# Performance work log

Hardware: AMD Instinct MI355X
Metric: run time of the kernel (lower is better)

Reference implementation:

```python
import jax, jax.numpy as jnp
import numpy as np

B, L, DIN, D, H, NL, DFF = 4, 1024, 64, 512, 8, 3, 2048
DH = D // H
N_RBF = 8
LARGE_NEG, CLAMP = 10000.0, 20.0


def layernorm(x, g, b, eps=1e-5):
    m = x.mean(-1, keepdims=True)
    v = x.var(-1, keepdims=True)
    return (x - m) * jax.lax.rsqrt(v + eps) * g + b


def sinusoidal_pe(length, d):
    pos = np.arange(length, dtype=np.float32)[:, None]
    div = np.exp(np.arange(0, d, 2, dtype=np.float32) * (-np.log(10000.0) / d))
    pe = np.zeros((length, d), dtype=np.float32)
    pe[:, 0::2] = np.sin(pos * div)
    pe[:, 1::2] = np.cos(pos * div)
    return jnp.asarray(pe)


def rbf(v):
    centers = jnp.linspace(0.0, 1.0, N_RBF)
    widths = jnp.full((N_RBF,), 0.2)
    diff = (v[..., None] - centers) / (widths + 1e-6)
    return jnp.exp(-0.5 * diff * diff)


def setup_inputs() -> dict:
    key = jax.random.key(0)
    ks = jax.random.split(key, 40)
    g = lambda k, shape: (jax.random.normal(k, shape) * 0.02).astype(jnp.float32)
    feat_dim = D + 2 + 2 * N_RBF  # base PE + raw(2) + 2 RBFs
    inp = {
        "x": jax.random.normal(ks[0], (B, L, DIN), jnp.float32),
        "lengths": jax.random.randint(ks[1], (B,), L // 2, L + 1),
        "input_delay": jax.random.uniform(ks[2], (B,), jnp.float32),
        "c_local": jax.random.uniform(ks[3], (B, L), jnp.float32).at[:, 0].set(0.0),
        "c_sink": jax.random.uniform(ks[4], (B, L), jnp.float32),
        # input projection
        "in_w": g(ks[5], (D, DIN)), "in_b": jnp.zeros((D,)),
        # delay encoder: Linear(1,D) -> GELU -> Linear(D,D) -> LN
        "de_w1": g(ks[6], (D, 1)), "de_b1": jnp.zeros((D,)),
        "de_w2": g(ks[7], (D, D)), "de_b2": jnp.zeros((D,)),
        "de_ln_g": jnp.ones((D,)), "de_ln_b": jnp.zeros((D,)),
        # corr positional encoding
        "cpe_w": g(ks[8], (D, feat_dim)), "cpe_b": jnp.zeros((D,)),
        "cpe_ln_g": jnp.ones((D,)), "cpe_ln_b": jnp.zeros((D,)),
        "gain": jnp.float32(0.5),
        # bias params
        "alpha": jnp.float32(10.0), "beta": jnp.float32(10.0),
        "floor": jnp.float32(0.1), "gamma": jnp.float32(0.7),
        # per-layer stacks
        "inproj_w": g(ks[9], (NL, 3 * D, D)), "inproj_b": jnp.zeros((NL, 3 * D)),
        "outproj_w": g(ks[10], (NL, D, D)), "outproj_b": jnp.zeros((NL, D)),
        "ln1_g": jnp.ones((NL, D)), "ln1_b": jnp.zeros((NL, D)),
        "ln2_g": jnp.ones((NL, D)), "ln2_b": jnp.zeros((NL, D)),
        "ff_w1": g(ks[11], (NL, DFF, D)), "ff_b1": jnp.zeros((NL, DFF)),
        "ff_w2": g(ks[12], (NL, D, DFF)), "ff_b2": jnp.zeros((NL, D)),
        "out_ln_g": jnp.ones((D,)), "out_ln_b": jnp.zeros((D,)),
    }
    return inp


def _forward(x, input_delay, c_local, c_sink, in_w, in_b, de_w1, de_b1, de_w2, de_b2,
             de_ln_g, de_ln_b, cpe_w, cpe_b, cpe_ln_g, cpe_ln_b, gain, alpha, beta,
             floor, gamma, inproj_w, inproj_b, outproj_w, outproj_b, ln1_g, ln1_b,
             ln2_g, ln2_b, ff_w1, ff_b1, ff_w2, ff_b2, out_ln_g, out_ln_b, lengths):
    Bc, Lc, _ = x.shape
    mask = jnp.arange(Lc)[None, :] >= lengths[:, None]          # [B,L] True=pad

    # input projection
    h = x @ in_w.T + in_b

    # delay feature encoder
    e = input_delay[:, None] @ de_w1.T + de_b1
    e = jax.nn.gelu(e, approximate=False) @ de_w2.T + de_b2
    e = layernorm(e, de_ln_g, de_ln_b)
    h = h + e[:, None, :]

    # corr positional encoding (uses clamped correlations)
    cl = jnp.clip(c_local, 0.0, 1.0)
    cs = jnp.clip(c_sink, 0.0, 1.0)
    pe_base = jnp.broadcast_to(sinusoidal_pe(Lc, D)[None], (Bc, Lc, D))
    z = jnp.concatenate([pe_base, jnp.stack([cl, cs], -1), rbf(cl), rbf(cs)], axis=-1)
    pe = layernorm(z @ cpe_w.T + cpe_b, cpe_ln_g, cpe_ln_b)
    pe = gain * pe
    pe = jnp.where(mask[..., None], 0.0, pe)
    h = h + pe

    # neighbor-correlation attention bias [B,1,L,L] (identical across layers/heads)
    idx = jnp.arange(Lc)
    neigh = jnp.abs(idx[None, :] - idx[:, None]) == 1           # [L,L]
    c_edge = jnp.zeros((Bc, Lc, Lc), x.dtype)
    c_edge = c_edge.at[:, 1:, :-1].set(jnp.broadcast_to(c_local[:, 1:, None], (Bc, Lc - 1, Lc - 1)))
    c_edge = c_edge.at[:, :-1, 1:].set(jnp.broadcast_to(c_local[:, None, 1:], (Bc, Lc - 1, Lc - 1)))
    bias = alpha * jnp.where(neigh[None], c_edge, 0.0)
    bias = jnp.where(mask[:, :, None] | mask[:, None, :], 0.0, bias)

    # sink bias (row 0 only): floor + (1-floor)*(c_sink^gamma)
    c_remap = floor + (1.0 - floor) * jnp.power(cs + 1e-6, gamma)
    sink_row = beta * jnp.where(mask, 0.0, c_remap)             # [B,L]
    attn_bias = bias[:, None].at[:, :, 0, :].add(sink_row[:, None, :])  # [B,1,L,L]

    pad = mask[:, None, None, :].astype(x.dtype)                # [B,1,1,L]
    scale = 1.0 / (DH ** 0.5)

    for i in range(NL):
        hn = layernorm(h, ln1_g[i], ln1_b[i])
        qkv = hn @ inproj_w[i].T + inproj_b[i]                  # [B,L,3D]
        q, k, v = jnp.split(qkv, 3, axis=-1)
        q = q.reshape(Bc, Lc, H, DH).transpose(0, 2, 1, 3)      # [B,H,L,d]
        k = k.reshape(Bc, Lc, H, DH).transpose(0, 2, 1, 3)
        v = v.reshape(Bc, Lc, H, DH).transpose(0, 2, 1, 3)
        scores = jnp.einsum('bhqd,bhkd->bhqk', q, k) * scale + attn_bias
        scores = scores - LARGE_NEG * pad
        scores = scores - scores.max(axis=-1, keepdims=True)
        scores = jnp.clip(scores, -CLAMP, CLAMP)
        attn = jax.nn.softmax(scores, axis=-1)
        o = jnp.einsum('bhqk,bhkd->bhqd', attn, v)
        o = o.transpose(0, 2, 1, 3).reshape(Bc, Lc, D)
        h = h + (o @ outproj_w[i].T + outproj_b[i])
        hn2 = layernorm(h, ln2_g[i], ln2_b[i])
        ff = jax.nn.gelu(hn2 @ ff_w1[i].T + ff_b1[i], approximate=False)
        h = h + (ff @ ff_w2[i].T + ff_b2[i])

    return layernorm(h, out_ln_g, out_ln_b)


def reference(x, lengths, input_delay, c_local, c_sink, in_w, in_b, de_w1, de_b1,
              de_w2, de_b2, de_ln_g, de_ln_b, cpe_w, cpe_b, cpe_ln_g, cpe_ln_b, gain,
              alpha, beta, floor, gamma, inproj_w, inproj_b, outproj_w, outproj_b,
              ln1_g, ln1_b, ln2_g, ln2_b, ff_w1, ff_b1, ff_w2, ff_b2, out_ln_g, out_ln_b):
    return _forward(x, input_delay, c_local, c_sink, in_w, in_b, de_w1, de_b1, de_w2,
                    de_b2, de_ln_g, de_ln_b, cpe_w, cpe_b, cpe_ln_g, cpe_ln_b, gain,
                    alpha, beta, floor, gamma, inproj_w, inproj_b, outproj_w,
                    outproj_b, ln1_g, ln1_b, ln2_g, ln2_b, ff_w1, ff_b1, ff_w2, ff_b2,
                    out_ln_g, out_ln_b, lengths)
```

## Files before the change

kernel.cpp:

```cpp
#include <hip/hip_runtime.h>
#include <math.h>

#define BB 4
#define LL 1024
#define DIN 64
#define DD 512
#define HH 8
#define DH 64
#define NLAYER 3
#define DFF 2048
#define FEAT 530
#define FEATP 544
#define MM 4096

typedef float f32x4 __attribute__((ext_vector_type(4)));
typedef short s16x8 __attribute__((ext_vector_type(8)));

__device__ __forceinline__ unsigned short f2bf(float f) {
    unsigned int u = __float_as_uint(f);
    u += 0x7fffu + ((u >> 16) & 1u);
    return (unsigned short)(u >> 16);
}
__device__ __forceinline__ float bf2f(unsigned short u) {
    return __uint_as_float(((unsigned int)u) << 16);
}
__device__ __forceinline__ float gelu_exact(float x) {
    return 0.5f * x * (1.0f + erff(x * 0.7071067811865475f));
}
__device__ __forceinline__ float wave_reduce_sum(float v) {
    #pragma unroll
    for (int o = 32; o; o >>= 1) v += __shfl_down(v, o);
    return v;
}
__device__ __forceinline__ void gload16(const unsigned short* g, unsigned short* l) {
    __builtin_amdgcn_global_load_lds(
        (const __attribute__((address_space(1))) unsigned int*)g,
        (__attribute__((address_space(3))) unsigned int*)l, 16, 0, 0);
}

__global__ __launch_bounds__(256) void cvt_kernel(
    const float* __restrict__ in, unsigned short* __restrict__ out, int n)
{
    for (int i = blockIdx.x * 256 + threadIdx.x; i < n; i += gridDim.x * 256)
        out[i] = f2bf(in[i]);
}

__global__ __launch_bounds__(256) void cpe_pad_kernel(
    const float* __restrict__ in, unsigned short* __restrict__ out)
{
    for (int i = blockIdx.x * 256 + threadIdx.x; i < DD * FEATP; i += gridDim.x * 256) {
        int r = i / FEATP, c = i - r * FEATP;
        out[i] = (c < FEAT) ? f2bf(in[(size_t)r * FEAT + c]) : 0;
    }
}

__global__ __launch_bounds__(256) void build_z_kernel(
    const float* __restrict__ c_local, const float* __restrict__ c_sink,
    unsigned short* __restrict__ Z)
{
    int row = blockIdx.x;
    int b = row >> 10, l = row & 1023;
    int t = threadIdx.x;
    unsigned short* zr = Z + (size_t)row * FEATP;
    for (int d = t; d < DD; d += 256) {
        int i = d >> 1;
        float dv = expf((float)(2 * i) * (-0.017988946135618352f));
        float ang = (float)l * dv;
        zr[d] = f2bf((d & 1) ? cosf(ang) : sinf(ang));
    }
    if (t < 32) {
        float cl = c_local[(size_t)b * LL + l]; cl = fminf(fmaxf(cl, 0.f), 1.f);
        float cs = c_sink [(size_t)b * LL + l]; cs = fminf(fmaxf(cs, 0.f), 1.f);
        float v = 0.f;
        if (t == 0) v = cl;
        else if (t == 1) v = cs;
        else if (t < 10)  { float c = (float)(t - 2) * (1.0f / 7.0f);  float df = (cl - c) / 0.200001f; v = expf(-0.5f * df * df); }
        else if (t < 18)  { float c = (float)(t - 10) * (1.0f / 7.0f); float df = (cs - c) / 0.200001f; v = expf(-0.5f * df * df); }
        zr[512 + t] = (t < 18) ? f2bf(v) : 0;
    }
}

__global__ __launch_bounds__(256) void sink_kernel(
    const float* __restrict__ c_sink, const int* __restrict__ lengths,
    const float* __restrict__ beta_p, const float* __restrict__ floor_p,
    const float* __restrict__ gamma_p, float* __restrict__ srow)
{
    int i = blockIdx.x * 256 + threadIdx.x;
    int b = i >> 10, k = i & 1023;
    float beta = *beta_p, flr = *floor_p, gmm = *gamma_p;
    float cs = c_sink[i]; cs = fminf(fmaxf(cs, 0.f), 1.f);
    float v = beta * (flr + (1.f - flr) * powf(cs + 1e-6f, gmm));
    srow[i] = (k < lengths[b]) ? v : 0.f;
}

__global__ __launch_bounds__(512) void delay_kernel(
    const float* __restrict__ delay, const float* __restrict__ w1, const float* __restrict__ b1,
    const float* __restrict__ w2, const float* __restrict__ b2,
    const float* __restrict__ lng, const float* __restrict__ lnb,
    float* __restrict__ e)
{
    int b = blockIdx.x;
    int t = threadIdx.x;
    __shared__ float g1[DD];
    __shared__ float red[16];
    float t1 = delay[b] * w1[t] + b1[t];
    g1[t] = gelu_exact(t1);
    __syncthreads();
    const float* wr = w2 + (size_t)t * DD;
    float s = b2[t];
    for (int j = 0; j < DD; j += 4) {
        float4 w4 = *(const float4*)(wr + j);
        s += w4.x * g1[j] + w4.y * g1[j+1] + w4.z * g1[j+2] + w4.w * g1[j+3];
    }
    float rs = wave_reduce_sum(s);
    float rss = wave_reduce_sum(s * s);
    int lane = t & 63, w = t >> 6;
    if (lane == 0) { red[w] = rs; red[8 + w] = rss; }
    __syncthreads();
    float mean = 0.f, msq = 0.f;
    #pragma unroll
    for (int i = 0; i < 8; ++i) { mean += red[i]; msq += red[8 + i]; }
    mean *= (1.0f / DD); msq *= (1.0f / DD);
    float rstd = rsqrtf(msq - mean * mean + 1e-5f);
    e[(size_t)b * DD + t] = (s - mean) * rstd * lng[t] + lnb[t];
}

template<int BM, int BN, int FM, int FN, int WGN, int MODE>
__global__ __launch_bounds__(256) void gemm_t(
    const unsigned short* __restrict__ A, const unsigned short* __restrict__ W,
    const float* __restrict__ bias, const float* __restrict__ resid,
    float* __restrict__ outf, unsigned short* __restrict__ outb,
    int M, int N, int K)
{
    __shared__ __align__(16) unsigned short As[BM * 32];
    __shared__ __align__(16) unsigned short Ws[BN * 32];
    int bm = blockIdx.y * BM, bn = blockIdx.x * BN;
    int t = threadIdx.x;
    int lane = t & 63, wid = t >> 6;
    int wr = wid / WGN, wc = wid % WGN;
    int l15 = lane & 15, lg = lane >> 4;
    int srow = lane >> 2;
    int sc8 = ((lane & 3) ^ ((lane >> 2) & 3) ^ ((lane >> 4) & 3)) * 8;
    int chunk8 = (lg ^ (l15 & 3) ^ ((l15 >> 2) & 3)) * 8;

    f32x4 acc[FM][FN] = {};
    int nk = K >> 5;

    for (int ks = 0; ks < nk; ++ks) {
        int kb = ks * 32;
        #pragma unroll
        for (int i = 0; i < BM / 64; ++i) {
            int row = wid * (BM / 4) + i * 16 + srow;
            gload16(A + (size_t)(bm + row) * K + kb + sc8, &As[(wid * (BM / 64) + i) * 512]);
        }
        #pragma unroll
        for (int i = 0; i < BN / 64; ++i) {
            int row = wid * (BN / 4) + i * 16 + srow;
            gload16(W + (size_t)(bn + row) * K + kb + sc8, &Ws[(wid * (BN / 64) + i) * 512]);
        }
        __syncthreads();
        s16x8 af[FM], wf[FN];
        #pragma unroll
        for (int mi = 0; mi < FM; ++mi)
            af[mi] = *(const s16x8*)&As[(wr * FM * 16 + mi * 16 + l15) * 32 + chunk8];
        #pragma unroll
        for (int ni = 0; ni < FN; ++ni)
            wf[ni] = *(const s16x8*)&Ws[(wc * FN * 16 + ni * 16 + l15) * 32 + chunk8];
        #pragma unroll
        for (int mi = 0; mi < FM; ++mi)
            #pragma unroll
            for (int ni = 0; ni < FN; ++ni)
                acc[mi][ni] = __builtin_amdgcn_mfma_f32_16x16x32_bf16(af[mi], wf[ni], acc[mi][ni], 0, 0, 0);
        __syncthreads();
    }

    int rbase = (lane >> 4) * 4;
    #pragma unroll
    for (int mi = 0; mi < FM; ++mi) {
        #pragma unroll
        for (int ni = 0; ni < FN; ++ni) {
            int n = bn + wc * FN * 16 + ni * 16 + l15;
            float bz = bias[n];
            #pragma unroll
            for (int r2 = 0; r2 < 4; ++r2) {
                int m = bm + wr * FM * 16 + mi * 16 + rbase + r2;
                float v = acc[mi][ni][r2] + bz;
                size_t o = (size_t)m * N + n;
                if (MODE == 0)      outf[o] = v;
                else if (MODE == 1) outb[o] = f2bf(v);
                else if (MODE == 2) outf[o] = v + resid[o];
                else                outb[o] = f2bf(gelu_exact(v));
            }
        }
    }
}

__global__ __launch_bounds__(256) void vtrans_kernel(
    const unsigned short* __restrict__ qkv, unsigned short* __restrict__ Vt)
{
    __shared__ unsigned short Ts[64 * 68];
    int l0 = blockIdx.x * 64;
    int hh = blockIdx.y;
    int b  = blockIdx.z;
    int t  = threadIdx.x;
    #pragma unroll
    for (int u = 0; u < 2; ++u) {
        int idx = t + u * 256;
        int r = idx >> 3, c8 = idx & 7;
        uint4 v = *(const uint4*)(qkv + (size_t)(b * LL + l0 + r) * 1536 + 1024 + hh * DH + c8 * 8);
        *(uint4*)&Ts[r * 68 + c8 * 8] = v;
    }
    __syncthreads();
    #pragma unroll
    for (int u = 0; u < 2; ++u) {
        int d = (t >> 3) + u * 32;
        int c = t & 7;
        unsigned short tmp[8];
        #pragma unroll
        for (int j = 0; j < 8; ++j) tmp[j] = Ts[(c * 8 + j) * 68 + d];
        *(uint4*)(Vt + ((size_t)((b * HH + hh) * DH + d)) * LL + l0 + c * 8) = *(const uint4*)tmp;
    }
}

#define SK 72
#define SPB 72
__global__ __launch_bounds__(256) void attn_mfma(
    const unsigned short* __restrict__ qkv, const unsigned short* __restrict__ Vt,
    const float* __restrict__ c_local, const float* __restrict__ srow,
    const int* __restrict__ lengths,
    const float* __restrict__ alpha_p,
    unsigned short* __restrict__ o)
{
    __shared__ __align__(16) unsigned short Ks[64 * SK];
    __shared__ __align__(16) unsigned short Vts[64 * SK];
    __shared__ __align__(16) unsigned short Psb[64 * SPB];

    int id = blockIdx.x;
    int swz = (id & 7) * 64 + (id >> 3);
    int q0 = (swz & 15) * 64;
    int hh = (swz >> 4) & 7;
    int b  = swz >> 7;

    int t  = threadIdx.x;
    int lane = t & 63, w = t >> 6;
    int l15 = lane & 15, lg = lane >> 4;
    int len = lengths[b];
    int nt = (len + 63) >> 6;
    const float alpha = *alpha_p;

    const unsigned short* qrow = qkv + (size_t)(b * LL + q0 + w * 16 + l15) * 1536 + hh * DH;
    s16x8 qf0 = *(const s16x8*)(qrow + lg * 8);
    s16x8 qf1 = *(const s16x8*)(qrow + 32 + lg * 8);
    #pragma unroll
    for (int j = 0; j < 8; ++j) {
        qf0[j] = (short)f2bf(bf2f((unsigned short)qf0[j]) * 0.125f);
        qf1[j] = (short)f2bf(bf2f((unsigned short)qf1[j]) * 0.125f);
    }

    float cm1[4], cp1[4];
    #pragma unroll
    for (int r2 = 0; r2 < 4; ++r2) {
        int qi = q0 + w * 16 + lg * 4 + r2;
        cm1[r2] = 0.f; cp1[r2] = 0.f;
        if (qi >= 1 && qi < len) {
            int src = (qi == 1 || qi == LL - 1) ? qi : qi - 1;
            cm1[r2] = alpha * c_local[(size_t)b * LL + src];
        }
        if (qi + 1 < LL && qi < len)
            cp1[r2] = alpha * c_local[(size_t)b * LL + qi + 1];
    }
    bool need_sink = (q0 == 0 && w == 0 && lg == 0);

    float m_run[4], l_run[4];
    f32x4 accO[4] = {};
    #pragma unroll
    for (int r2 = 0; r2 < 4; ++r2) { m_run[r2] = -1e30f; l_run[r2] = 0.f; }

    int sr = t >> 3, sc8 = (t & 7) * 8;
    const unsigned short* kbase = qkv + (size_t)(b * LL) * 1536 + 512 + hh * DH;
    const unsigned short* vbase = Vt + ((size_t)((b * HH + hh) * DH)) * LL;

    uint4 pk0 = *(const uint4*)(kbase + (size_t)sr * 1536 + sc8);
    uint4 pk1 = *(const uint4*)(kbase + (size_t)(sr + 32) * 1536 + sc8);
    uint4 pv0 = *(const uint4*)(vbase + (size_t)sr * LL + sc8);
    uint4 pv1 = *(const uint4*)(vbase + (size_t)(sr + 32) * LL + sc8);

    for (int kt = 0; kt < nt; ++kt) {
        int k0 = kt * 64;
        *(uint4*)&Ks[sr * SK + sc8]         = pk0;
        *(uint4*)&Ks[(sr + 32) * SK + sc8]  = pk1;
        *(uint4*)&Vts[sr * SK + sc8]        = pv0;
        *(uint4*)&Vts[(sr + 32) * SK + sc8] = pv1;
        if (kt + 1 < nt) {
            int kn = k0 + 64;
            pk0 = *(const uint4*)(kbase + (size_t)(kn + sr) * 1536 + sc8);
            pk1 = *(const uint4*)(kbase + (size_t)(kn + sr + 32) * 1536 + sc8);
            pv0 = *(const uint4*)(vbase + (size_t)sr * LL + kn + sc8);
            pv1 = *(const uint4*)(vbase + (size_t)(sr + 32) * LL + kn + sc8);
        }
        __syncthreads();

        f32x4 accS[4] = {};
        #pragma unroll
        for (int ct = 0; ct < 4; ++ct) {
            s16x8 kf0 = *(const s16x8*)&Ks[(ct * 16 + l15) * SK + lg * 8];
            s16x8 kf1 = *(const s16x8*)&Ks[(ct * 16 + l15) * SK + 32 + lg * 8];
            accS[ct] = __builtin_amdgcn_mfma_f32_16x16x32_bf16(qf0, kf0, accS[ct], 0, 0, 0);
            accS[ct] = __builtin_amdgcn_mfma_f32_16x16x32_bf16(qf1, kf1, accS[ct], 0, 0, 0);
        }

        float m4[4] = { -1e30f, -1e30f, -1e30f, -1e30f };
        if (k0 + 64 <= len) {
            #pragma unroll
            for (int ct = 0; ct < 4; ++ct) {
                int k = k0 + ct * 16 + l15;
                float sink_ct = need_sink ? srow[(size_t)b * LL + k] : 0.f;
                #pragma unroll
                for (int r2 = 0; r2 < 4; ++r2) {
                    int qi = q0 + w * 16 + lg * 4 + r2;
                    float v = accS[ct][r2];
                    if (k == qi - 1) v += cm1[r2];
                    else if (k == qi + 1) v += cp1[r2];
                    if (r2 == 0) v += sink_ct;
                    accS[ct][r2] = v;
                    m4[r2] = fmaxf(m4[r2], v);
                }
            }
        } else {
            #pragma unroll
            for (int ct = 0; ct < 4; ++ct) {
                int k = k0 + ct * 16 + l15;
                bool maskk = (k >= len);
                float sink_ct = need_sink ? srow[(size_t)b * LL + k] : 0.f;
                #pragma unroll
                for (int r2 = 0; r2 < 4; ++r2) {
                    int qi = q0 + w * 16 + lg * 4 + r2;
                    float v = accS[ct][r2];
                    if (k == qi - 1) v += cm1[r2];
                    else if (k == qi + 1 && !maskk) v += cp1[r2];
                    if (r2 == 0) v += sink_ct;
                    if (maskk) v -= 10000.f;
                    accS[ct][r2] = v;
                    m4[r2] = fmaxf(m4[r2], v);
                }
            }
        }

        #pragma unroll
        for (int r2 = 0; r2 < 4; ++r2) {
            #pragma unroll
            for (int msk = 1; msk < 16; msk <<= 1) m4[r2] = fmaxf(m4[r2], __shfl_xor(m4[r2], msk));
            float mnew = fmaxf(m_run[r2], m4[r2]);
            float scl = __expf(m_run[r2] - mnew);
            m_run[r2] = mnew;
            float rowsum = 0.f;
            #pragma unroll
            for (int ct = 0; ct < 4; ++ct) {
                float p = __expf(accS[ct][r2] - mnew);
                rowsum += p;
                Psb[(w * 16 + lg * 4 + r2) * SPB + ct * 16 + l15] = f2bf(p);
            }
            #pragma unroll
            for (int msk = 1; msk < 16; msk <<= 1) rowsum += __shfl_xor(rowsum, msk);
            l_run[r2] = l_run[r2] * scl + rowsum;
            #pragma unroll
            for (int dt = 0; dt < 4; ++dt) accO[dt][r2] *= scl;
        }

        #pragma unroll
        for (int kk = 0; kk < 2; ++kk) {
            s16x8 pf = *(const s16x8*)&Psb[(w * 16 + l15) * SPB + kk * 32 + lg * 8];
            #pragma unroll
            for (int dt = 0; dt < 4; ++dt) {
                s16x8 vf = *(const s16x8*)&Vts[(dt * 16 + l15) * SK + kk * 32 + lg * 8];
                accO[dt] = __builtin_amdgcn_mfma_f32_16x16x32_bf16(pf, vf, accO[dt], 0, 0, 0);
            }
        }
        __syncthreads();
    }

    #pragma unroll
    for (int r2 = 0; r2 < 4; ++r2) {
        float inv = 1.f / l_run[r2];
        int qi = q0 + w * 16 + lg * 4 + r2;
        #pragma unroll
        for (int dt = 0; dt < 4; ++dt)
            o[(size_t)(b * LL + qi) * DD + hh * DH + dt * 16 + l15] = f2bf(accO[dt][r2] * inv);
    }
}

__global__ __launch_bounds__(256) void embed_ep_kernel(
    const float* __restrict__ cpe_pre, const float* __restrict__ e,
    const int* __restrict__ lengths,
    const float* __restrict__ cpe_g, const float* __restrict__ cpe_lb,
    const float* __restrict__ gain_p, float* __restrict__ h)
{
    int row = blockIdx.x;
    int b = row >> 10, l = row & 1023;
    int t = threadIdx.x;
    __shared__ float red[16];
    const float* cp = cpe_pre + (size_t)row * DD;
    float v0 = cp[t], v1 = cp[t + 256];
    float s = v0 + v1, ss = v0 * v0 + v1 * v1;
    float rs = wave_reduce_sum(s), rss = wave_reduce_sum(ss);
    int lane = t & 63, w = t >> 6;
    if (lane == 0) { red[w] = rs; red[8 + w] = rss; }
    __syncthreads();
    float mean = 0.f, msq = 0.f;
    #pragma unroll
    for (int i = 0; i < 4; ++i) { mean += red[i]; msq += red[8 + i]; }
    mean *= (1.0f / DD); msq *= (1.0f / DD);
    float rstd = rsqrtf(msq - mean * mean + 1e-5f);
    bool maskp = (l >= lengths[b]);
    float gain = *gain_p;
    float pe0 = maskp ? 0.f : gain * ((v0 - mean) * rstd * cpe_g[t] + cpe_lb[t]);
    float pe1 = maskp ? 0.f : gain * ((v1 - mean) * rstd * cpe_g[t + 256] + cpe_lb[t + 256]);
    h[(size_t)row * DD + t]       += e[(size_t)b * DD + t] + pe0;
    h[(size_t)row * DD + t + 256] += e[(size_t)b * DD + t + 256] + pe1;
}

__global__ __launch_bounds__(256) void ln_kernel(
    const float* __restrict__ in, float* __restrict__ out,
    const float* __restrict__ g, const float* __restrict__ bta)
{
    int row = blockIdx.x; int t = threadIdx.x;
    __shared__ float red[16];
    const float* xr = in + (size_t)row * DD;
    float2 v = ((const float2*)xr)[t];
    float s = v.x + v.y, ss = v.x * v.x + v.y * v.y;
    float rs = wave_reduce_sum(s), rss = wave_reduce_sum(ss);
    int lane = t & 63, w = t >> 6;
    if (lane == 0) { red[w] = rs; red[8 + w] = rss; }
    __syncthreads();
    float mean = 0.f, msq = 0.f;
    #pragma unroll
    for (int i = 0; i < 4; ++i) { mean += red[i]; msq += red[8 + i]; }
    mean *= (1.0f / DD); msq *= (1.0f / DD);
    float rstd = rsqrtf(msq - mean * mean + 1e-5f);
    float2 gg = ((const float2*)g)[t], bb = ((const float2*)bta)[t];
    float2 o;
    o.x = (v.x - mean) * rstd * gg.x + bb.x;
    o.y = (v.y - mean) * rstd * gg.y + bb.y;
    ((float2*)(out + (size_t)row * DD))[t] = o;
}

__global__ __launch_bounds__(256) void ln_bf16_kernel(
    const float* __restrict__ in, unsigned short* __restrict__ out,
    const float* __restrict__ g, const float* __restrict__ bta)
{
    int row = blockIdx.x; int t = threadIdx.x;
    __shared__ float red[16];
    const float* xr = in + (size_t)row * DD;
    float2 v = ((const float2*)xr)[t];
    float s = v.x + v.y, ss = v.x * v.x + v.y * v.y;
    float rs = wave_reduce_sum(s), rss = wave_reduce_sum(ss);
    int lane = t & 63, w = t >> 6;
    if (lane == 0) { red[w] = rs; red[8 + w] = rss; }
    __syncthreads();
    float mean = 0.f, msq = 0.f;
    #pragma unroll
    for (int i = 0; i < 4; ++i) { mean += red[i]; msq += red[8 + i]; }
    mean *= (1.0f / DD); msq *= (1.0f / DD);
    float rstd = rsqrtf(msq - mean * mean + 1e-5f);
    float2 gg = ((const float2*)g)[t], bb = ((const float2*)bta)[t];
    ushort2 o;
    o.x = f2bf((v.x - mean) * rstd * gg.x + bb.x);
    o.y = f2bf((v.y - mean) * rstd * gg.y + bb.y);
    ((ushort2*)(out + (size_t)row * DD))[t] = o;
}

extern "C" void kernel_launch(void* const* d_in, const int* in_sizes, int n_in,
                              void* d_out, int out_size, void* d_ws, size_t ws_size,
                              hipStream_t stream)
{
    const float* x          = (const float*)d_in[0];
    const int*   lengths    = (const int*)  d_in[1];
    const float* input_delay= (const float*)d_in[2];
    const float* c_local    = (const float*)d_in[3];
    const float* c_sink     = (const float*)d_in[4];
    const float* in_w       = (const float*)d_in[5];
    const float* in_b       = (const float*)d_in[6];
    const float* de_w1      = (const float*)d_in[7];
    const float* de_b1      = (const float*)d_in[8];
    const float* de_w2      = (const float*)d_in[9];
    const float* de_b2      = (const float*)d_in[10];
    const float* de_ln_g    = (const float*)d_in[11];
    const float* de_ln_b    = (const float*)d_in[12];
    const float* cpe_w      = (const float*)d_in[13];
    const float* cpe_b      = (const float*)d_in[14];
    const float* cpe_ln_g   = (const float*)d_in[15];
    const float* cpe_ln_b   = (const float*)d_in[16];
    const float* gain       = (const float*)d_in[17];
    const float* alpha      = (const float*)d_in[18];
    const float* beta       = (const float*)d_in[19];
    const float* floorp     = (const float*)d_in[20];
    const float* gammap     = (const float*)d_in[21];
    const float* inproj_w   = (const float*)d_in[22];
    const float* inproj_b   = (const float*)d_in[23];
    const float* outproj_w  = (const float*)d_in[24];
    const float* outproj_b  = (const float*)d_in[25];
    const float* ln1_g      = (const float*)d_in[26];
    const float* ln1_b      = (const float*)d_in[27];
    const float* ln2_g      = (const float*)d_in[28];
    const float* ln2_b      = (const float*)d_in[29];
    const float* ff_w1      = (const float*)d_in[30];
    const float* ff_b1      = (const float*)d_in[31];
    const float* ff_w2      = (const float*)d_in[32];
    const float* ff_b2      = (const float*)d_in[33];
    const float* out_ln_g   = (const float*)d_in[34];
    const float* out_ln_b   = (const float*)d_in[35];

    char* base = (char*)d_ws;
    float* h            = (float*)base;
    unsigned short* act1 = (unsigned short*)(base + 8u*1024*1024);
    char* bigb          = base + 12u*1024*1024;
    unsigned short* qkvb = (unsigned short*)bigb;
    unsigned short* vtb  = (unsigned short*)(bigb + 12u*1024*1024);
    unsigned short* ffb  = (unsigned short*)bigb;
    unsigned short* Zb   = (unsigned short*)bigb;
    unsigned short* x_bf = (unsigned short*)(bigb + 5u*1024*1024);
    float* cpe_pre       = (float*)(bigb + 8u*1024*1024);
    unsigned short* w_inproj  = (unsigned short*)(base + 28u*1024*1024);
    unsigned short* w_outproj = w_inproj  + (size_t)3*1536*512;
    unsigned short* w_ff1     = w_outproj + (size_t)3*512*512;
    unsigned short* w_ff2     = w_ff1     + (size_t)3*2048*512;
    unsigned short* w_in      = w_ff2     + (size_t)3*512*2048;
    unsigned short* w_cpe     = w_in      + (size_t)512*64;
    float* e                  = (float*)(w_cpe + (size_t)512*544);
    float* srow               = e + (size_t)BB*DD;

    cvt_kernel<<<128, 256, 0, stream>>>(x, x_bf, MM * DIN);
    cvt_kernel<<<2048, 256, 0, stream>>>(inproj_w, w_inproj, 3 * 1536 * 512);
    cvt_kernel<<<1024, 256, 0, stream>>>(outproj_w, w_outproj, 3 * 512 * 512);
    cvt_kernel<<<2048, 256, 0, stream>>>(ff_w1, w_ff1, 3 * 2048 * 512);
    cvt_kernel<<<2048, 256, 0, stream>>>(ff_w2, w_ff2, 3 * 512 * 2048);
    cvt_kernel<<<64, 256, 0, stream>>>(in_w, w_in, 512 * 64);
    cpe_pad_kernel<<<1024, 256, 0, stream>>>(cpe_w, w_cpe);

    delay_kernel<<<BB, 512, 0, stream>>>(input_delay, de_w1, de_b1, de_w2, de_b2, de_ln_g, de_ln_b, e);
    build_z_kernel<<<MM, 256, 0, stream>>>(c_local, c_sink, Zb);
    sink_kernel<<<BB * LL / 256, 256, 0, stream>>>(c_sink, lengths, beta, floorp, gammap, srow);

    gemm_t<64, 64, 2, 2, 2, 0><<<dim3(DD / 64, MM / 64), 256, 0, stream>>>(
        x_bf, w_in, in_b, nullptr, h, nullptr, MM, DD, DIN);
    gemm_t<64, 64, 2, 2, 2, 0><<<dim3(DD / 64, MM / 64), 256, 0, stream>>>(
        Zb, w_cpe, cpe_b, nullptr, cpe_pre, nullptr, MM, DD, FEATP);
    embed_ep_kernel<<<MM, 256, 0, stream>>>(cpe_pre, e, lengths, cpe_ln_g, cpe_ln_b, gain, h);

    for (int i = 0; i < NLAYER; ++i) {
        ln_bf16_kernel<<<MM, 256, 0, stream>>>(h, act1, ln1_g + (size_t)i * DD, ln1_b + (size_t)i * DD);
        gemm_t<64, 128, 2, 4, 2, 1><<<dim3(1536 / 128, MM / 64), 256, 0, stream>>>(
            act1, w_inproj + (size_t)i * 1536 * 512, inproj_b + (size_t)i * 1536,
            nullptr, nullptr, qkvb, MM, 1536, DD);
        vtrans_kernel<<<dim3(LL / 64, HH, BB), 256, 0, stream>>>(qkvb, vtb);
        attn_mfma<<<512, 256, 0, stream>>>(qkvb, vtb, c_local, srow, lengths, alpha, act1);
        gemm_t<64, 64, 2, 2, 2, 2><<<dim3(DD / 64, MM / 64), 256, 0, stream>>>(
            act1, w_outproj + (size_t)i * 512 * 512, outproj_b + (size_t)i * DD,
            h, h, nullptr, MM, DD, DD);
        ln_bf16_kernel<<<MM, 256, 0, stream>>>(h, act1, ln2_g + (size_t)i * DD, ln2_b + (size_t)i * DD);
        gemm_t<128, 128, 4, 4, 2, 3><<<dim3(DFF / 128, MM / 128), 256, 0, stream>>>(
            act1, w_ff1 + (size_t)i * 2048 * 512, ff_b1 + (size_t)i * DFF,
            nullptr, nullptr, ffb, MM, DFF, DD);
        gemm_t<64, 64, 2, 2, 2, 2><<<dim3(DD / 64, MM / 64), 256, 0, stream>>>(
            ffb, w_ff2 + (size_t)i * 512 * 2048, ff_b2 + (size_t)i * DD,
            h, h, nullptr, MM, DD, DFF);
    }
    ln_kernel<<<MM, 256, 0, stream>>>(h, (float*)d_out, out_ln_g, out_ln_b);
}
```

Baseline: 484.8 us.

## Compute V transposed directly via swapped GEMM and add fast path for attention bias

The fused QKV projection is split into a Q/K GEMM and a separate V GEMM whose operands are swapped (W_v × act^T), so V is written directly in a transposed [d, B*L] layout. This removes the standalone vtrans kernel and its extra global round trip. A new GEMM epilogue mode applies the bias per row. The attention kernel also gains a fast path that skips the per-element local/sink bias checks on key tiles that cannot touch the diagonal neighbours or the sink row. The cost is an extra GEMM launch with a smaller N for Q/K, plus more branching in the attention loop.

```diff
diff --git a/kernel.cpp b/kernel.cpp
--- a/kernel.cpp
+++ b/kernel.cpp
@@ -180,52 +180,26 @@
         #pragma unroll
         for (int ni = 0; ni < FN; ++ni) {
             int n = bn + wc * FN * 16 + ni * 16 + l15;
-            float bz = bias[n];
+            float bzc = (MODE == 4) ? 0.f : bias[n];
             #pragma unroll
             for (int r2 = 0; r2 < 4; ++r2) {
                 int m = bm + wr * FM * 16 + mi * 16 + rbase + r2;
-                float v = acc[mi][ni][r2] + bz;
+                float v = acc[mi][ni][r2] + ((MODE == 4) ? bias[m] : bzc);
                 size_t o = (size_t)m * N + n;
                 if (MODE == 0)      outf[o] = v;
                 else if (MODE == 1) outb[o] = f2bf(v);
                 else if (MODE == 2) outf[o] = v + resid[o];
-                else                outb[o] = f2bf(gelu_exact(v));
+                else if (MODE == 3) outb[o] = f2bf(gelu_exact(v));
+                else                outb[o] = f2bf(v);
             }
         }
-    }
-}
-
-__global__ __launch_bounds__(256) void vtrans_kernel(
-    const unsigned short* __restrict__ qkv, unsigned short* __restrict__ Vt)
-{
-    __shared__ unsigned short Ts[64 * 68];
-    int l0 = blockIdx.x * 64;
-    int hh = blockIdx.y;
-    int b  = blockIdx.z;
-    int t  = threadIdx.x;
-    #pragma unroll
-    for (int u = 0; u < 2; ++u) {
-        int idx = t + u * 256;
-        int r = idx >> 3, c8 = idx & 7;
-        uint4 v = *(const uint4*)(qkv + (size_t)(b * LL + l0 + r) * 1536 + 1024 + hh * DH + c8 * 8);
-        *(uint4*)&Ts[r * 68 + c8 * 8] = v;
-    }
-    __syncthreads();
-    #pragma unroll
-    for (int u = 0; u < 2; ++u) {
-        int d = (t >> 3) + u * 32;
-        int c = t & 7;
-        unsigned short tmp[8];
-        #pragma unroll
-        for (int j = 0; j < 8; ++j) tmp[j] = Ts[(c * 8 + j) * 68 + d];
-        *(uint4*)(Vt + ((size_t)((b * HH + hh) * DH + d)) * LL + l0 + c * 8) = *(const uint4*)tmp;
     }
 }
 
 #define SK 72
 #define SPB 72
 __global__ __launch_bounds__(256) void attn_mfma(
-    const unsigned short* __restrict__ qkv, const unsigned short* __restrict__ Vt,
+    const unsigned short* __restrict__ qk, const unsigned short* __restrict__ Vt,
     const float* __restrict__ c_local, const float* __restrict__ srow,
     const int* __restrict__ lengths,
     const float* __restrict__ alpha_p,
@@ -246,9 +220,11 @@
     int l15 = lane & 15, lg = lane >> 4;
     int len = lengths[b];
     int nt = (len + 63) >> 6;
+    int kt0 = q0 >> 6;
+    bool sink_blk = (q0 == 0);
     const float alpha = *alpha_p;
 
-    const unsigned short* qrow = qkv + (size_t)(b * LL + q0 + w * 16 + l15) * 1536 + hh * DH;
+    const unsigned short* qrow = qk + (size_t)(b * LL + q0 + w * 16 + l15) * 1024 + hh * DH;
     s16x8 qf0 = *(const s16x8*)(qrow + lg * 8);
     s16x8 qf1 = *(const s16x8*)(qrow + 32 + lg * 8);
     #pragma unroll
@@ -269,7 +245,7 @@
         if (qi + 1 < LL && qi < len)
             cp1[r2] = alpha * c_local[(size_t)b * LL + qi + 1];
     }
-    bool need_sink = (q0 == 0 && w == 0 && lg == 0);
+    bool need_sink = (sink_blk && w == 0 && lg == 0);
 
     float m_run[4], l_run[4];
     f32x4 accO[4] = {};
@@ -277,13 +253,13 @@
     for (int r2 = 0; r2 < 4; ++r2) { m_run[r2] = -1e30f; l_run[r2] = 0.f; }
 
     int sr = t >> 3, sc8 = (t & 7) * 8;
-    const unsigned short* kbase = qkv + (size_t)(b * LL) * 1536 + 512 + hh * DH;
-    const unsigned short* vbase = Vt + ((size_t)((b * HH + hh) * DH)) * LL;
-
-    uint4 pk0 = *(const uint4*)(kbase + (size_t)sr * 1536 + sc8);
-    uint4 pk1 = *(const uint4*)(kbase + (size_t)(sr + 32) * 1536 + sc8);
-    uint4 pv0 = *(const uint4*)(vbase + (size_t)sr * LL + sc8);
-    uint4 pv1 = *(const uint4*)(vbase + (size_t)(sr + 32) * LL + sc8);
+    const unsigned short* kbase = qk + (size_t)(b * LL) * 1024 + 512 + hh * DH;
+    const unsigned short* vbase = Vt + (size_t)(hh * DH) * MM + b * LL;
+
+    uint4 pk0 = *(const uint4*)(kbase + (size_t)sr * 1024 + sc8);
+    uint4 pk1 = *(const uint4*)(kbase + (size_t)(sr + 32) * 1024 + sc8);
+    uint4 pv0 = *(const uint4*)(vbase + (size_t)sr * MM + sc8);
+    uint4 pv1 = *(const uint4*)(vbase + (size_t)(sr + 32) * MM + sc8);
 
     for (int kt = 0; kt < nt; ++kt) {
         int k0 = kt * 64;
@@ -293,10 +269,10 @@
         *(uint4*)&Vts[(sr + 32) * SK + sc8] = pv1;
         if (kt + 1 < nt) {
             int kn = k0 + 64;
-            pk0 = *(const uint4*)(kbase + (size_t)(kn + sr) * 1536 + sc8);
-            pk1 = *(const uint4*)(kbase + (size_t)(kn + sr + 32) * 1536 + sc8);
-            pv0 = *(const uint4*)(vbase + (size_t)sr * LL + kn + sc8);
-            pv1 = *(const uint4*)(vbase + (size_t)(sr + 32) * LL + kn + sc8);
+            pk0 = *(const uint4*)(kbase + (size_t)(kn + sr) * 1024 + sc8);
+            pk1 = *(const uint4*)(kbase + (size_t)(kn + sr + 32) * 1024 + sc8);
+            pv0 = *(const uint4*)(vbase + (size_t)sr * MM + kn + sc8);
+            pv1 = *(const uint4*)(vbase + (size_t)(sr + 32) * MM + kn + sc8);
         }
         __syncthreads();
 
@@ -310,7 +286,14 @@
         }
 
         float m4[4] = { -1e30f, -1e30f, -1e30f, -1e30f };
-        if (k0 + 64 <= len) {
+        bool slow = sink_blk || (kt >= kt0 - 1 && kt <= kt0 + 1) || (k0 + 64 > len);
+        if (!slow) {
+            #pragma unroll
+            for (int ct = 0; ct < 4; ++ct)
+                #pragma unroll
+                for (int r2 = 0; r2 < 4; ++r2)
+                    m4[r2] = fmaxf(m4[r2], accS[ct][r2]);
+        } else if (k0 + 64 <= len) {
             #pragma unroll
             for (int ct = 0; ct < 4; ++ct) {
                 int k = k0 + ct * 16 + l15;
@@ -514,7 +497,7 @@
     float* h            = (float*)base;
     unsigned short* act1 = (unsigned short*)(base + 8u*1024*1024);
     char* bigb          = base + 12u*1024*1024;
-    unsigned short* qkvb = (unsigned short*)bigb;
+    unsigned short* qkb  = (unsigned short*)bigb;
     unsigned short* vtb  = (unsigned short*)(bigb + 12u*1024*1024);
     unsigned short* ffb  = (unsigned short*)bigb;
     unsigned short* Zb   = (unsigned short*)bigb;
@@ -548,12 +531,14 @@
     embed_ep_kernel<<<MM, 256, 0, stream>>>(cpe_pre, e, lengths, cpe_ln_g, cpe_ln_b, gain, h);
 
     for (int i = 0; i < NLAYER; ++i) {
+        const unsigned short* wqk = w_inproj + (size_t)i * 1536 * 512;
+        const unsigned short* wv  = wqk + (size_t)1024 * 512;
         ln_bf16_kernel<<<MM, 256, 0, stream>>>(h, act1, ln1_g + (size_t)i * DD, ln1_b + (size_t)i * DD);
-        gemm_t<64, 128, 2, 4, 2, 1><<<dim3(1536 / 128, MM / 64), 256, 0, stream>>>(
-            act1, w_inproj + (size_t)i * 1536 * 512, inproj_b + (size_t)i * 1536,
-            nullptr, nullptr, qkvb, MM, 1536, DD);
-        vtrans_kernel<<<dim3(LL / 64, HH, BB), 256, 0, stream>>>(qkvb, vtb);
-        attn_mfma<<<512, 256, 0, stream>>>(qkvb, vtb, c_local, srow, lengths, alpha, act1);
+        gemm_t<64, 128, 2, 4, 2, 1><<<dim3(1024 / 128, MM / 64), 256, 0, stream>>>(
+            act1, wqk, inproj_b + (size_t)i * 1536, nullptr, nullptr, qkb, MM, 1024, DD);
+        gemm_t<64, 64, 2, 2, 2, 4><<<dim3(MM / 64, DD / 64), 256, 0, stream>>>(
+            wv, act1, inproj_b + (size_t)i * 1536 + 1024, nullptr, nullptr, vtb, DD, MM, DD);
+        attn_mfma<<<512, 256, 0, stream>>>(qkb, vtb, c_local, srow, lengths, alpha, act1);
         gemm_t<64, 64, 2, 2, 2, 2><<<dim3(DD / 64, MM / 64), 256, 0, stream>>>(
             act1, w_outproj + (size_t)i * 512 * 512, outproj_b + (size_t)i * DD,
             h, h, nullptr, MM, DD, DD);
```

Result: no change. 491.4 us (+1.4%).
